# Kernel tuning notes

Hardware: AMD Instinct MI355X
Metric: run time of the kernel (lower is better)

## Reference

```python
import jax, jax.numpy as jnp
import numpy as np

HIDDEN = 768
NUM_BLOCKS = 8
BLOCK = HIDDEN // NUM_BLOCKS  # 96
HSF = 1                       # hidden_size_factor
LAMBDA = 0.01                 # softshrink threshold
SCALE = 0.02


def setup_inputs() -> dict:
    key = jax.random.key(0)
    ks = jax.random.split(key, 9)
    B, C, N = 16, HIDDEN, 4096
    x = jax.random.normal(ks[0], (B, C, N), dtype=jnp.float32)
    u = lambda k, shp: SCALE * jax.random.uniform(k, shp, dtype=jnp.float32)
    OB = BLOCK * HSF
    return {
        'x': x,
        'w1_re': u(ks[1], (NUM_BLOCKS, BLOCK, OB)),
        'w1_im': u(ks[2], (NUM_BLOCKS, BLOCK, OB)),
        'w2_re': u(ks[3], (NUM_BLOCKS, OB, BLOCK)),
        'w2_im': u(ks[4], (NUM_BLOCKS, OB, BLOCK)),
        'b1_re': u(ks[5], (NUM_BLOCKS, OB)),
        'b1_im': u(ks[6], (NUM_BLOCKS, OB)),
        'b2_re': u(ks[7], (NUM_BLOCKS, BLOCK)),
        'b2_im': u(ks[8], (NUM_BLOCKS, BLOCK)),
    }


def _softshrink(v, lam):
    return jnp.sign(v) * jnp.maximum(jnp.abs(v) - lam, 0.0)


def _crelu(z):
    # activation applied to view_as_real, i.e. independently on re/im
    return jax.lax.complex(jnp.maximum(z.real, 0.0), jnp.maximum(z.imag, 0.0))


def reference(x, w1_re, w1_im, w2_re, w2_im, b1_re, b1_im, b2_re, b2_im):
    B, C, N = x.shape
    bias = x
    w1 = jax.lax.complex(w1_re, w1_im)
    w2 = jax.lax.complex(w2_re, w2_im)
    b1 = jax.lax.complex(b1_re, b1_im)
    b2 = jax.lax.complex(b2_re, b2_im)

    xf = jnp.fft.rfft(x.astype(jnp.float32), norm='ortho')   # [B, C, M], M = N//2+1
    M = xf.shape[-1]
    xf = xf.reshape(B, NUM_BLOCKS, BLOCK, M)                  # [B, nb, bs, M]

    # kept_modes == M since hard_thresholding_fraction == 1
    h = jnp.einsum('bnim,nio->bnom', xf, w1) + b1[None, :, :, None]
    h = _crelu(h)
    o = jnp.einsum('bnim,nio->bnom', h, w2) + b2[None, :, :, None]
    o = jax.lax.complex(_softshrink(o.real, LAMBDA), _softshrink(o.imag, LAMBDA))

    o = o.reshape(B, C, M)
    y = jnp.fft.irfft(o, n=N, norm='ortho').astype(x.dtype)
    return y + bias
```

## Files before the change

kernel.cpp:

```cpp
#include <hip/hip_runtime.h>
#include <math.h>

#define NTH 256
#define LAM 0.01f
#define WS_WT_BYTES 589824

typedef __attribute__((ext_vector_type(8))) short short8;
typedef __attribute__((ext_vector_type(8))) unsigned short ushort8;
typedef __attribute__((ext_vector_type(4))) float f32x4;
typedef __attribute__((ext_vector_type(4))) unsigned int uint4v;

__device__ __forceinline__ ushort f2bf(float f) {
    union { float f; unsigned u; } c; c.f = f;
    unsigned u = c.u;
    u += 0x7fffu + ((u >> 16) & 1u);
    return (ushort)(u >> 16);
}
__device__ __forceinline__ float bf2f(ushort h) {
    union { unsigned u; float f; } c; c.u = ((unsigned)h) << 16; return c.f;
}


__device__ __forceinline__ int pad(int i) { return i + (i >> 3); }
#define FFT_LDS_SZ 2304

__device__ __forceinline__ float2 cadd(float2 a, float2 b) { return make_float2(a.x + b.x, a.y + b.y); }
__device__ __forceinline__ float2 csub(float2 a, float2 b) { return make_float2(a.x - b.x, a.y - b.y); }
__device__ __forceinline__ float2 cmul(float2 a, float2 b) { return make_float2(a.x * b.x - a.y * b.y, a.x * b.y + a.y * b.x); }
__device__ __forceinline__ float2 cjrot(float2 a, float sign) { return make_float2(-sign * a.y, sign * a.x); }

__device__ __forceinline__ void radix8_bfly(const float2 t[8], float2 o[8], float sign) {
    float2 apc = cadd(t[0], t[4]), amc = csub(t[0], t[4]);
    float2 bpd = cadd(t[2], t[6]), bmd = csub(t[2], t[6]);
    float2 e0 = cadd(apc, bpd), e2 = csub(apc, bpd);
    float2 jb = cjrot(bmd, sign);
    float2 e1 = cadd(amc, jb), e3 = csub(amc, jb);
    float2 apc2 = cadd(t[1], t[5]), amc2 = csub(t[1], t[5]);
    float2 bpd2 = cadd(t[3], t[7]), bmd2 = csub(t[3], t[7]);
    float2 q0 = cadd(apc2, bpd2), q2 = csub(apc2, bpd2);
    float2 jb2 = cjrot(bmd2, sign);
    float2 q1 = cadd(amc2, jb2), q3 = csub(amc2, jb2);
    const float H = 0.70710678118654752f;
    q1 = cmul(q1, make_float2(H, sign * H));
    q2 = cjrot(q2, sign);
    q3 = cmul(q3, make_float2(-H, sign * H));
    o[0] = cadd(e0, q0); o[1] = cadd(e1, q1); o[2] = cadd(e2, q2); o[3] = cadd(e3, q3);
    o[4] = csub(e0, q0); o[5] = csub(e1, q1); o[6] = csub(e2, q2); o[7] = csub(e3, q3);
}

__device__ __forceinline__ void radix8_stage(const float2* __restrict__ src,
                                             float2* __restrict__ dst,
                                             int tid, int Ns, float sign) {
    const int u = tid;
    const int r = u & (Ns - 1);
    float2 t[8];
    t[0] = src[pad(u)];
    t[1] = src[pad(u + 256)];
    t[2] = src[pad(u + 512)];
    t[3] = src[pad(u + 768)];
    t[4] = src[pad(u + 1024)];
    t[5] = src[pad(u + 1280)];
    t[6] = src[pad(u + 1536)];
    t[7] = src[pad(u + 1792)];
    {
        float ang = sign * ((float)M_PI / (4.0f * (float)Ns)) * (float)r;
        float s1, c1;
        __sincosf(ang, &s1, &c1);
        float2 w1 = make_float2(c1, s1);
        float2 w2 = cmul(w1, w1);
        float2 w3 = cmul(w2, w1);
        float2 w4 = cmul(w2, w2);
        float2 w5 = cmul(w4, w1);
        float2 w6 = cmul(w4, w2);
        float2 w7 = cmul(w4, w3);
        t[1] = cmul(t[1], w1); t[2] = cmul(t[2], w2); t[3] = cmul(t[3], w3);
        t[4] = cmul(t[4], w4); t[5] = cmul(t[5], w5); t[6] = cmul(t[6], w6);
        t[7] = cmul(t[7], w7);
    }
    float2 o[8];
    radix8_bfly(t, o, sign);
    const int d = ((u - r) << 3) + r;
    dst[pad(d)]          = o[0];
    dst[pad(d + Ns)]     = o[1];
    dst[pad(d + 2 * Ns)] = o[2];
    dst[pad(d + 3 * Ns)] = o[3];
    dst[pad(d + 4 * Ns)] = o[4];
    dst[pad(d + 5 * Ns)] = o[5];
    dst[pad(d + 6 * Ns)] = o[6];
    dst[pad(d + 7 * Ns)] = o[7];
}

__device__ __forceinline__ void radix4_final(const float2* __restrict__ src,
                                             float2* __restrict__ dst,
                                             int tid, float sign) {
    for (int u = tid; u < 512; u += NTH) {
        float2 x0 = src[pad(u)];
        float2 x1 = src[pad(u + 512)];
        float2 x2 = src[pad(u + 1024)];
        float2 x3 = src[pad(u + 1536)];
        float ang = sign * ((float)M_PI / 1024.0f) * (float)u;
        float s1, c1;
        __sincosf(ang, &s1, &c1);
        float2 w1 = make_float2(c1, s1);
        float2 w2 = cmul(w1, w1);
        float2 w3 = cmul(w2, w1);
        x1 = cmul(x1, w1); x2 = cmul(x2, w2); x3 = cmul(x3, w3);
        float2 apc = cadd(x0, x2), amc = csub(x0, x2);
        float2 bpd = cadd(x1, x3), bmd = csub(x1, x3);
        float2 e = cjrot(bmd, sign);
        dst[pad(u)]        = cadd(apc, bpd);
        dst[pad(u + 512)]  = cadd(amc, e);
        dst[pad(u + 1024)] = csub(apc, bpd);
        dst[pad(u + 1536)] = csub(amc, e);
    }
}

__global__ __launch_bounds__(NTH, 4) void k_rfft_fwd(const float* __restrict__ x,
                                                     float* __restrict__ out) {
    __shared__ float2 bufA[FFT_LDS_SZ];
    __shared__ float2 bufB[FFT_LDS_SZ];
    const int row = blockIdx.x;
    const float* xr = x + (size_t)row * 4096;
    unsigned* srow = (unsigned*)(out + (size_t)row * 4096);
    const int tid = threadIdx.x;

    {
        float2 t[8], o[8];
#pragma unroll
        for (int j = 0; j < 8; ++j)
            t[j] = *(const float2*)(xr + 2 * (tid + 256 * j));
        radix8_bfly(t, o, -1.0f);
#pragma unroll
        for (int j = 0; j < 8; ++j)
            bufB[pad(8 * tid + j)] = o[j];
    }
    __syncthreads();
    radix8_stage(bufB, bufA, tid, 8, -1.0f);
    __syncthreads();
    radix8_stage(bufA, bufB, tid, 64, -1.0f);
    __syncthreads();
    radix4_final(bufB, bufA, tid, -1.0f);
    __syncthreads();
    float2* Z = bufA;

    const float scale = 1.0f / 64.0f;
    float s0, c0;
    __sincosf(-(float)M_PI * (float)tid / 2048.0f, &s0, &c0);
    float2 w = make_float2(c0, s0);
    const float2 stepw = make_float2(0.92387953251128674f, -0.38268343236508978f);
    for (int k = tid; k <= 2048; k += NTH) {
        float2 zk = Z[pad(k & 2047)];
        float2 zn = Z[pad((2048 - k) & 2047)];
        float Ar = 0.5f * (zk.x + zn.x), Ai = 0.5f * (zk.y - zn.y);
        float Br = 0.5f * (zk.x - zn.x), Bi = 0.5f * (zk.y + zn.y);
        float wBr = w.x * Br - w.y * Bi;
        float wBi = w.x * Bi + w.y * Br;
        float Xr = (Ar + wBi) * scale;
        float Xi = (Ai - wBr) * scale;
        if (k == 0)          ((ushort*)srow)[0] = f2bf(Xr);
        else if (k == 2048)  ((ushort*)srow)[1] = f2bf(Xr);
        else                 srow[k] = (unsigned)f2bf(Xr) | ((unsigned)f2bf(Xi) << 16);
        w = cmul(w, stepw);
    }
}

__global__ __launch_bounds__(NTH) void k_prep(
    const float* __restrict__ w1_re, const float* __restrict__ w1_im,
    const float* __restrict__ w2_re, const float* __restrict__ w2_im,
    ushort* __restrict__ wt) {
    int gid = blockIdx.x * NTH + threadIdx.x;
    if (gid >= 294912) return;
    int a   = gid / 73728;
    int rem = gid - a * 73728;
    int n   = rem / 9216;
    int r2  = rem - n * 9216;
    int o   = r2 / 96;
    int i   = r2 - o * 96;
    const float* src = (a == 0) ? w1_re : (a == 1) ? w1_im : (a == 2) ? w2_re : w2_im;
    wt[gid] = f2bf(src[(n * 96 + i) * 96 + o]);
}

__global__ __launch_bounds__(NTH, 3) void k_mix6(
    float* __restrict__ io, const ushort* __restrict__ wt,
    const float* __restrict__ b1_re, const float* __restrict__ b1_im,
    const float* __restrict__ b2_re, const float* __restrict__ b2_im) {
    __shared__ __align__(16) ushort xb[2][64][104];

    const int mt = blockIdx.x;
    const int n  = blockIdx.y;
    const int b  = blockIdx.z;
    const int tid  = threadIdx.x;
    const int lane = tid & 63;
    const int wv   = tid >> 6;
    const int m0 = mt * 64;
    const int mw = wv * 16;
    unsigned* sb = (unsigned*)(io + ((size_t)b * 768 + (size_t)n * 96) * 4096);

    const int lc = lane & 15;
    const int hi = lane >> 4;

    {
        const int m = m0 + mw + lc;
        if (m >= 1 && m < 2048) {
            const unsigned* src0 = sb + m;
#pragma unroll
            for (int half = 0; half < 2; ++half) {
                unsigned v[12];
#pragma unroll
                for (int t = 0; t < 12; ++t) {
                    const int i = hi + 4 * (12 * half + t);
                    v[t] = src0[(size_t)i * 4096];
                }
#pragma unroll
                for (int t = 0; t < 12; ++t) {
                    const int i = hi + 4 * (12 * half + t);
                    xb[0][mw + lc][i] = (ushort)v[t];
                    xb[1][mw + lc][i] = (ushort)(v[t] >> 16);
                }
            }
        } else {
            for (int i = hi; i < 96; i += 4) {
                const ushort* rw = (const ushort*)(sb + (size_t)i * 4096);
                ushort re16 = 0;
                if (m == 0)          re16 = rw[0];
                else if (m == 2048)  re16 = rw[1];
                xb[0][mw + lc][i] = re16;
                xb[1][mw + lc][i] = 0;
            }
        }
    }

    const int kl = 8 * hi;
    const int mrow = mw + lc;
    const ushort* wn  = wt + (size_t)n * 9216;
    const ushort* wn2 = wn + 2 * 73728;

    float b1r[6], b1i[6];
#pragma unroll
    for (int nt = 0; nt < 6; ++nt) {
        b1r[nt] = b1_re[n * 96 + nt * 16 + lc];
        b1i[nt] = b1_im[n * 96 + nt * 16 + lc];
    }

    f32x4 accR[6], accI[6];
    const f32x4 zero = {0.f, 0.f, 0.f, 0.f};
#pragma unroll
    for (int nt = 0; nt < 6; ++nt) { accR[nt] = zero; accI[nt] = zero; }

#pragma unroll
    for (int kk = 0; kk < 3; ++kk) {
        const int k0 = kk * 32 + kl;
        short8 wr[6], wi[6];
#pragma unroll
        for (int nt = 0; nt < 6; ++nt) {
            const ushort* wp = wn + (nt * 16 + lc) * 96 + k0;
            wr[nt] = *(const short8*)(wp);
            wi[nt] = *(const short8*)(wp + 73728);
        }
        short8 ar = *(const short8*)&xb[0][mrow][k0];
        short8 ai = *(const short8*)&xb[1][mrow][k0];
        short8 nai;
#pragma unroll
        for (int j = 0; j < 8; ++j) nai[j] = ai[j] ^ (short)0x8000;
#pragma unroll
        for (int nt = 0; nt < 6; ++nt) {
            accR[nt] = __builtin_amdgcn_mfma_f32_16x16x32_bf16(ar,  wr[nt], accR[nt], 0, 0, 0);
            accR[nt] = __builtin_amdgcn_mfma_f32_16x16x32_bf16(nai, wi[nt], accR[nt], 0, 0, 0);
            accI[nt] = __builtin_amdgcn_mfma_f32_16x16x32_bf16(ar,  wi[nt], accI[nt], 0, 0, 0);
            accI[nt] = __builtin_amdgcn_mfma_f32_16x16x32_bf16(ai,  wr[nt], accI[nt], 0, 0, 0);
        }
    }
#pragma unroll
    for (int nt = 0; nt < 6; ++nt) {
#pragma unroll
        for (int q = 0; q < 4; ++q) {
            int m = mw + 4 * hi + q;
            xb[0][m][nt * 16 + lc] = f2bf(fmaxf(accR[nt][q] + b1r[nt], 0.f));
            xb[1][m][nt * 16 + lc] = f2bf(fmaxf(accI[nt][q] + b1i[nt], 0.f));
        }
    }

#pragma unroll
    for (int nt = 0; nt < 6; ++nt) { accR[nt] = zero; accI[nt] = zero; }
#pragma unroll
    for (int kk = 0; kk < 3; ++kk) {
        const int k0 = kk * 32 + kl;
        short8 wr[6], wi[6];
#pragma unroll
        for (int nt = 0; nt < 6; ++nt) {
            const ushort* wp = wn2 + (nt * 16 + lc) * 96 + k0;
            wr[nt] = *(const short8*)(wp);
            wi[nt] = *(const short8*)(wp + 73728);
        }
        short8 ar = *(const short8*)&xb[0][mrow][k0];
        short8 ai = *(const short8*)&xb[1][mrow][k0];
        short8 nai;
#pragma unroll
        for (int j = 0; j < 8; ++j) nai[j] = ai[j] ^ (short)0x8000;
#pragma unroll
        for (int nt = 0; nt < 6; ++nt) {
            accR[nt] = __builtin_amdgcn_mfma_f32_16x16x32_bf16(ar,  wr[nt], accR[nt], 0, 0, 0);
            accR[nt] = __builtin_amdgcn_mfma_f32_16x16x32_bf16(nai, wi[nt], accR[nt], 0, 0, 0);
            accI[nt] = __builtin_amdgcn_mfma_f32_16x16x32_bf16(ar,  wi[nt], accI[nt], 0, 0, 0);
            accI[nt] = __builtin_amdgcn_mfma_f32_16x16x32_bf16(ai,  wr[nt], accI[nt], 0, 0, 0);
        }
    }

    float b2r[6], b2i[6];
#pragma unroll
    for (int nt = 0; nt < 6; ++nt) {
        b2r[nt] = b2_re[n * 96 + nt * 16 + lc];
        b2i[nt] = b2_im[n * 96 + nt * 16 + lc];
    }
    const int mq = m0 + mw + 4 * hi;
#pragma unroll
    for (int nt = 0; nt < 6; ++nt) {
        float sr[4], si[4];
#pragma unroll
        for (int q = 0; q < 4; ++q) {
            float vr = accR[nt][q] + b2r[nt];
            float vi = accI[nt][q] + b2i[nt];
            sr[q] = copysignf(fmaxf(fabsf(vr) - LAM, 0.f), vr);
            si[q] = copysignf(fmaxf(fabsf(vi) - LAM, 0.f), vi);
        }
        unsigned* row = sb + (size_t)(nt * 16 + lc) * 4096;
        if (mq >= 1 && mq + 3 < 2048) {
            uint4v pk;
#pragma unroll
            for (int q = 0; q < 4; ++q)
                pk[q] = (unsigned)f2bf(sr[q]) | ((unsigned)f2bf(si[q]) << 16);
            *(uint4v*)(row + mq) = pk;
        } else {
#pragma unroll
            for (int q = 0; q < 4; ++q) {
                int m = mq + q;
                if (m == 0)          ((ushort*)row)[0] = f2bf(sr[q]);
                else if (m == 2048)  ((ushort*)row)[1] = f2bf(sr[q]);
                else if (m < 2048)   row[m] = (unsigned)f2bf(sr[q]) | ((unsigned)f2bf(si[q]) << 16);
            }
        }
    }
}

__global__ __launch_bounds__(NTH) void k_mix_fallback(
    float* __restrict__ io,
    const float* __restrict__ w1_re, const float* __restrict__ w1_im,
    const float* __restrict__ w2_re, const float* __restrict__ w2_im,
    const float* __restrict__ b1_re, const float* __restrict__ b1_im,
    const float* __restrict__ b2_re, const float* __restrict__ b2_im) {
    __shared__ __align__(16) ushort xb[2][64][96];
    __shared__ __align__(16) ushort wb[2][96][104];

    const int mt = blockIdx.x;
    const int n  = blockIdx.y;
    const int b  = blockIdx.z;
    const int tid = threadIdx.x;
    const int lane = tid & 63;
    const int wv   = tid >> 6;
    const int m0 = mt * 64;
    unsigned* sb = (unsigned*)(io + ((size_t)b * 768 + (size_t)n * 96) * 4096);

    for (int idx = tid; idx < 96 * 64; idx += NTH) {
        int i = idx >> 6, mm = idx & 63;
        int m = m0 + mm;
        const unsigned* row = sb + (size_t)i * 4096;
        ushort re = 0, im = 0;
        if (m == 0) { re = ((const ushort*)row)[0]; }
        else if (m == 2048) { re = ((const ushort*)row)[1]; }
        else if (m < 2048) { unsigned v = row[m]; re = (ushort)v; im = (ushort)(v >> 16); }
        xb[0][mm][i] = re;
        xb[1][mm][i] = im;
    }
    const float* W1r = w1_re + (size_t)n * 9216;
    const float* W1i = w1_im + (size_t)n * 9216;
    for (int idx = tid; idx < 9216; idx += NTH) {
        int i = idx / 96, o = idx - i * 96;
        wb[0][o][i] = f2bf(W1r[idx]);
        wb[1][o][i] = f2bf(W1i[idx]);
    }
    const int lc = lane & 15;
    float b1r[6], b1i[6], b2r[6], b2i[6];
#pragma unroll
    for (int nt = 0; nt < 6; ++nt) {
        b1r[nt] = b1_re[n * 96 + nt * 16 + lc];
        b1i[nt] = b1_im[n * 96 + nt * 16 + lc];
        b2r[nt] = b2_re[n * 96 + nt * 16 + lc];
        b2i[nt] = b2_im[n * 96 + nt * 16 + lc];
    }
    __syncthreads();

    const int mw = wv * 16;
    const int klr = 8 * (lane >> 4);
    const int mrow = mw + lc;

    f32x4 accR[6], accI[6];
    const f32x4 zero = {0.f, 0.f, 0.f, 0.f};
#pragma unroll
    for (int nt = 0; nt < 6; ++nt) { accR[nt] = zero; accI[nt] = zero; }

#pragma unroll
    for (int kk = 0; kk < 3; ++kk) {
        int k0 = kk * 32 + klr;
        short8 ar = *(const short8*)&xb[0][mrow][k0];
        short8 ai = *(const short8*)&xb[1][mrow][k0];
        short8 nai;
#pragma unroll
        for (int j = 0; j < 8; ++j) nai[j] = ai[j] ^ (short)0x8000;
#pragma unroll
        for (int nt = 0; nt < 6; ++nt) {
            short8 br = *(const short8*)&wb[0][nt * 16 + lc][k0];
            short8 bi = *(const short8*)&wb[1][nt * 16 + lc][k0];
            accR[nt] = __builtin_amdgcn_mfma_f32_16x16x32_bf16(ar,  br, accR[nt], 0, 0, 0);
            accR[nt] = __builtin_amdgcn_mfma_f32_16x16x32_bf16(nai, bi, accR[nt], 0, 0, 0);
            accI[nt] = __builtin_amdgcn_mfma_f32_16x16x32_bf16(ar,  bi, accI[nt], 0, 0, 0);
            accI[nt] = __builtin_amdgcn_mfma_f32_16x16x32_bf16(ai,  br, accI[nt], 0, 0, 0);
        }
    }
#pragma unroll
    for (int nt = 0; nt < 6; ++nt) {
#pragma unroll
        for (int q = 0; q < 4; ++q) {
            int m = mw + 4 * (lane >> 4) + q;
            float hr = fmaxf(accR[nt][q] + b1r[nt], 0.f);
            float hi2 = fmaxf(accI[nt][q] + b1i[nt], 0.f);
            xb[0][m][nt * 16 + lc] = f2bf(hr);
            xb[1][m][nt * 16 + lc] = f2bf(hi2);
        }
    }
    __syncthreads();

    const float* W2r = w2_re + (size_t)n * 9216;
    const float* W2i = w2_im + (size_t)n * 9216;
    for (int idx = tid; idx < 9216; idx += NTH) {
        int i = idx / 96, o = idx - i * 96;
        wb[0][o][i] = f2bf(W2r[idx]);
        wb[1][o][i] = f2bf(W2i[idx]);
    }
    __syncthreads();

#pragma unroll
    for (int nt = 0; nt < 6; ++nt) { accR[nt] = zero; accI[nt] = zero; }
#pragma unroll
    for (int kk = 0; kk < 3; ++kk) {
        int k0 = kk * 32 + klr;
        short8 ar = *(const short8*)&xb[0][mrow][k0];
        short8 ai = *(const short8*)&xb[1][mrow][k0];
        short8 nai;
#pragma unroll
        for (int j = 0; j < 8; ++j) nai[j] = ai[j] ^ (short)0x8000;
#pragma unroll
        for (int nt = 0; nt < 6; ++nt) {
            short8 br = *(const short8*)&wb[0][nt * 16 + lc][k0];
            short8 bi = *(const short8*)&wb[1][nt * 16 + lc][k0];
            accR[nt] = __builtin_amdgcn_mfma_f32_16x16x32_bf16(ar,  br, accR[nt], 0, 0, 0);
            accR[nt] = __builtin_amdgcn_mfma_f32_16x16x32_bf16(nai, bi, accR[nt], 0, 0, 0);
            accI[nt] = __builtin_amdgcn_mfma_f32_16x16x32_bf16(ar,  bi, accI[nt], 0, 0, 0);
            accI[nt] = __builtin_amdgcn_mfma_f32_16x16x32_bf16(ai,  br, accI[nt], 0, 0, 0);
        }
    }
#pragma unroll
    for (int nt = 0; nt < 6; ++nt) {
#pragma unroll
        for (int q = 0; q < 4; ++q) {
            int m = m0 + mw + 4 * (lane >> 4) + q;
            float vr = accR[nt][q] + b2r[nt];
            float vi = accI[nt][q] + b2i[nt];
            float sr = copysignf(fmaxf(fabsf(vr) - LAM, 0.f), vr);
            float si = copysignf(fmaxf(fabsf(vi) - LAM, 0.f), vi);
            unsigned* row = sb + (size_t)(nt * 16 + lc) * 4096;
            if (m == 0)          ((ushort*)row)[0] = f2bf(sr);
            else if (m == 2048)  ((ushort*)row)[1] = f2bf(sr);
            else if (m < 2048)   row[m] = (unsigned)f2bf(sr) | ((unsigned)f2bf(si) << 16);
        }
    }
}

__global__ __launch_bounds__(NTH, 4) void k_irfft_add(const float* __restrict__ x,
                                                      float* __restrict__ io) {
    __shared__ float2 bufA[FFT_LDS_SZ];
    __shared__ float2 bufB[FFT_LDS_SZ];
    const int row = blockIdx.x;
    const float* xr = x + (size_t)row * 4096;
    float* orow = io + (size_t)row * 4096;
    const unsigned* srow = (const unsigned*)orow;
    const int tid = threadIdx.x;
    const float scale = 1.0f / 32.0f;

    {
        float2 t[8], o[8];
        float s0, c0;
        __sincosf((float)M_PI * (float)tid / 2048.0f, &s0, &c0);
        float2 w = make_float2(c0, s0);
        const float2 stepw = make_float2(0.92387953251128674f, 0.38268343236508978f);
#pragma unroll
        for (int j = 0; j < 8; ++j) {
            const int k = tid + 256 * j;
            float Xr, Xi, Yr, Yi;
            if (k == 0) {
                unsigned v0 = srow[0];
                Xr = bf2f((ushort)v0); Xi = 0.f;
                Yr = bf2f((ushort)(v0 >> 16)); Yi = 0.f;
            } else {
                unsigned a  = srow[k];
                unsigned bq = srow[2048 - k];
                Xr = bf2f((ushort)a);  Xi = bf2f((ushort)(a >> 16));
                Yr = bf2f((ushort)bq); Yi = bf2f((ushort)(bq >> 16));
            }
            float Fer = 0.5f * (Xr + Yr), Fei = 0.5f * (Xi - Yi);
            float Dr  = 0.5f * (Xr - Yr), Di  = 0.5f * (Xi + Yi);
            float For = w.x * Dr - w.y * Di;
            float Foi = w.x * Di + w.y * Dr;
            t[j] = make_float2((Fer - Foi) * scale, (Fei + For) * scale);
            w = cmul(w, stepw);
        }
        radix8_bfly(t, o, 1.0f);
#pragma unroll
        for (int j = 0; j < 8; ++j)
            bufB[pad(8 * tid + j)] = o[j];
    }
    __syncthreads();
    radix8_stage(bufB, bufA, tid, 8, 1.0f);
    __syncthreads();
    radix8_stage(bufA, bufB, tid, 64, 1.0f);
    __syncthreads();

#pragma unroll
    for (int it = 0; it < 2; ++it) {
        const int u = tid + 256 * it;
        float2 x0 = bufB[pad(u)];
        float2 x1 = bufB[pad(u + 512)];
        float2 x2 = bufB[pad(u + 1024)];
        float2 x3 = bufB[pad(u + 1536)];
        float ang = ((float)M_PI / 1024.0f) * (float)u;
        float s1, c1;
        __sincosf(ang, &s1, &c1);
        float2 w1 = make_float2(c1, s1);
        float2 w2 = cmul(w1, w1);
        float2 w3 = cmul(w2, w1);
        x1 = cmul(x1, w1); x2 = cmul(x2, w2); x3 = cmul(x3, w3);
        float2 apc = cadd(x0, x2), amc = csub(x0, x2);
        float2 bpd = cadd(x1, x3), bmd = csub(x1, x3);
        float2 e = cjrot(bmd, 1.0f);
        float2 y0 = cadd(apc, bpd);
        float2 y1 = cadd(amc, e);
        float2 y2 = csub(apc, bpd);
        float2 y3 = csub(amc, e);
        float2 xv0 = *(const float2*)(xr + 2 * u);
        float2 xv1 = *(const float2*)(xr + 2 * (u + 512));
        float2 xv2 = *(const float2*)(xr + 2 * (u + 1024));
        float2 xv3 = *(const float2*)(xr + 2 * (u + 1536));
        *(float2*)(orow + 2 * u)          = cadd(y0, xv0);
        *(float2*)(orow + 2 * (u + 512))  = cadd(y1, xv1);
        *(float2*)(orow + 2 * (u + 1024)) = cadd(y2, xv2);
        *(float2*)(orow + 2 * (u + 1536)) = cadd(y3, xv3);
    }
}

extern "C" void kernel_launch(void* const* d_in, const int* in_sizes, int n_in,
                              void* d_out, int out_size, void* d_ws, size_t ws_size,
                              hipStream_t stream) {
    const float* x     = (const float*)d_in[0];
    const float* w1_re = (const float*)d_in[1];
    const float* w1_im = (const float*)d_in[2];
    const float* w2_re = (const float*)d_in[3];
    const float* w2_im = (const float*)d_in[4];
    const float* b1_re = (const float*)d_in[5];
    const float* b1_im = (const float*)d_in[6];
    const float* b2_re = (const float*)d_in[7];
    const float* b2_im = (const float*)d_in[8];
    float* out = (float*)d_out;

    k_rfft_fwd<<<12288, NTH, 0, stream>>>(x, out);
    if (ws_size >= (size_t)WS_WT_BYTES) {
        ushort* wt = (ushort*)d_ws;
        k_prep<<<(294912 + NTH - 1) / NTH, NTH, 0, stream>>>(w1_re, w1_im, w2_re, w2_im, wt);
        k_mix6<<<dim3(33, 8, 16), NTH, 0, stream>>>(out, wt, b1_re, b1_im, b2_re, b2_im);
    } else {
        k_mix_fallback<<<dim3(33, 8, 16), NTH, 0, stream>>>(out, w1_re, w1_im, w2_re, w2_im,
                                                            b1_re, b1_im, b2_re, b2_im);
    }
    k_irfft_add<<<12288, NTH, 0, stream>>>(x, out);
}
```

Before: 263.6 us.

## Process three m-tiles per block with register prefetch of the next tile

```diff
diff --git a/kernel.cpp b/kernel.cpp
--- a/kernel.cpp
+++ b/kernel.cpp
@@ -180,56 +180,23 @@
     wt[gid] = f2bf(src[(n * 96 + i) * 96 + o]);
 }
 
-__global__ __launch_bounds__(NTH, 3) void k_mix6(
+__global__ __launch_bounds__(NTH, 3) void k_mix7(
     float* __restrict__ io, const ushort* __restrict__ wt,
     const float* __restrict__ b1_re, const float* __restrict__ b1_im,
     const float* __restrict__ b2_re, const float* __restrict__ b2_im) {
     __shared__ __align__(16) ushort xb[2][64][104];
 
-    const int mt = blockIdx.x;
+    const int gx = blockIdx.x;
     const int n  = blockIdx.y;
     const int b  = blockIdx.z;
     const int tid  = threadIdx.x;
     const int lane = tid & 63;
     const int wv   = tid >> 6;
-    const int m0 = mt * 64;
     const int mw = wv * 16;
     unsigned* sb = (unsigned*)(io + ((size_t)b * 768 + (size_t)n * 96) * 4096);
 
     const int lc = lane & 15;
     const int hi = lane >> 4;
-
-    {
-        const int m = m0 + mw + lc;
-        if (m >= 1 && m < 2048) {
-            const unsigned* src0 = sb + m;
-#pragma unroll
-            for (int half = 0; half < 2; ++half) {
-                unsigned v[12];
-#pragma unroll
-                for (int t = 0; t < 12; ++t) {
-                    const int i = hi + 4 * (12 * half + t);
-                    v[t] = src0[(size_t)i * 4096];
-                }
-#pragma unroll
-                for (int t = 0; t < 12; ++t) {
-                    const int i = hi + 4 * (12 * half + t);
-                    xb[0][mw + lc][i] = (ushort)v[t];
-                    xb[1][mw + lc][i] = (ushort)(v[t] >> 16);
-                }
-            }
-        } else {
-            for (int i = hi; i < 96; i += 4) {
-                const ushort* rw = (const ushort*)(sb + (size_t)i * 4096);
-                ushort re16 = 0;
-                if (m == 0)          re16 = rw[0];
-                else if (m == 2048)  re16 = rw[1];
-                xb[0][mw + lc][i] = re16;
-                xb[1][mw + lc][i] = 0;
-            }
-        }
-    }
-
     const int kl = 8 * hi;
     const int mrow = mw + lc;
     const ushort* wn  = wt + (size_t)n * 9216;
@@ -242,101 +209,137 @@
         b1i[nt] = b1_im[n * 96 + nt * 16 + lc];
     }
 
-    f32x4 accR[6], accI[6];
+    unsigned vA[24];
+    {
+        const int m = gx * 192 + mw + lc;
+        const unsigned* src0 = sb + ((m >= 1 && m < 2048) ? m : 0);
+#pragma unroll
+        for (int t = 0; t < 24; ++t)
+            vA[t] = src0[(size_t)(hi + 4 * t) * 4096];
+    }
+
     const f32x4 zero = {0.f, 0.f, 0.f, 0.f};
-#pragma unroll
-    for (int nt = 0; nt < 6; ++nt) { accR[nt] = zero; accI[nt] = zero; }
-
-#pragma unroll
-    for (int kk = 0; kk < 3; ++kk) {
-        const int k0 = kk * 32 + kl;
-        short8 wr[6], wi[6];
+
+#pragma unroll
+    for (int j = 0; j < 3; ++j) {
+        const int m0 = (gx * 3 + j) * 64;
+        const int m  = m0 + mw + lc;
+        {
+            const bool interior = (m >= 1 && m < 2048);
+#pragma unroll
+            for (int t = 0; t < 24; ++t) {
+                const int i = hi + 4 * t;
+                unsigned v = vA[t];
+                ushort lo = (ushort)v, h16 = (ushort)(v >> 16);
+                ushort re = (m == 2048) ? h16 : (m < 2048 ? lo : (ushort)0);
+                ushort im = interior ? h16 : (ushort)0;
+                xb[0][mw + lc][i] = re;
+                xb[1][mw + lc][i] = im;
+            }
+        }
+        if (j < 2) {
+            const int mn = m0 + 64 + mw + lc;
+            const unsigned* src0 = sb + ((mn >= 1 && mn < 2048) ? mn : 0);
+#pragma unroll
+            for (int t = 0; t < 24; ++t)
+                vA[t] = src0[(size_t)(hi + 4 * t) * 4096];
+        }
+
+        f32x4 accR[6], accI[6];
+#pragma unroll
+        for (int nt = 0; nt < 6; ++nt) { accR[nt] = zero; accI[nt] = zero; }
+
+#pragma unroll
+        for (int kk = 0; kk < 3; ++kk) {
+            const int k0 = kk * 32 + kl;
+            short8 wr[6], wi[6];
+#pragma unroll
+            for (int nt = 0; nt < 6; ++nt) {
+                const ushort* wp = wn + (nt * 16 + lc) * 96 + k0;
+                wr[nt] = *(const short8*)(wp);
+                wi[nt] = *(const short8*)(wp + 73728);
+            }
+            short8 ar = *(const short8*)&xb[0][mrow][k0];
+            short8 ai = *(const short8*)&xb[1][mrow][k0];
+            short8 nai;
+#pragma unroll
+            for (int jj = 0; jj < 8; ++jj) nai[jj] = ai[jj] ^ (short)0x8000;
+#pragma unroll
+            for (int nt = 0; nt < 6; ++nt) {
+                accR[nt] = __builtin_amdgcn_mfma_f32_16x16x32_bf16(ar,  wr[nt], accR[nt], 0, 0, 0);
+                accR[nt] = __builtin_amdgcn_mfma_f32_16x16x32_bf16(nai, wi[nt], accR[nt], 0, 0, 0);
+                accI[nt] = __builtin_amdgcn_mfma_f32_16x16x32_bf16(ar,  wi[nt], accI[nt], 0, 0, 0);
+                accI[nt] = __builtin_amdgcn_mfma_f32_16x16x32_bf16(ai,  wr[nt], accI[nt], 0, 0, 0);
+            }
+        }
 #pragma unroll
         for (int nt = 0; nt < 6; ++nt) {
-            const ushort* wp = wn + (nt * 16 + lc) * 96 + k0;
-            wr[nt] = *(const short8*)(wp);
-            wi[nt] = *(const short8*)(wp + 73728);
-        }
-        short8 ar = *(const short8*)&xb[0][mrow][k0];
-        short8 ai = *(const short8*)&xb[1][mrow][k0];
-        short8 nai;
-#pragma unroll
-        for (int j = 0; j < 8; ++j) nai[j] = ai[j] ^ (short)0x8000;
+#pragma unroll
+            for (int q = 0; q < 4; ++q) {
+                int mm = mw + 4 * hi + q;
+                xb[0][mm][nt * 16 + lc] = f2bf(fmaxf(accR[nt][q] + b1r[nt], 0.f));
+                xb[1][mm][nt * 16 + lc] = f2bf(fmaxf(accI[nt][q] + b1i[nt], 0.f));
+            }
+        }
+
+#pragma unroll
+        for (int nt = 0; nt < 6; ++nt) { accR[nt] = zero; accI[nt] = zero; }
+#pragma unroll
+        for (int kk = 0; kk < 3; ++kk) {
+            const int k0 = kk * 32 + kl;
+            short8 wr[6], wi[6];
+#pragma unroll
+            for (int nt = 0; nt < 6; ++nt) {
+                const ushort* wp = wn2 + (nt * 16 + lc) * 96 + k0;
+                wr[nt] = *(const short8*)(wp);
+                wi[nt] = *(const short8*)(wp + 73728);
+            }
+            short8 ar = *(const short8*)&xb[0][mrow][k0];
+            short8 ai = *(const short8*)&xb[1][mrow][k0];
+            short8 nai;
+#pragma unroll
+            for (int jj = 0; jj < 8; ++jj) nai[jj] = ai[jj] ^ (short)0x8000;
+#pragma unroll
+            for (int nt = 0; nt < 6; ++nt) {
+                accR[nt] = __builtin_amdgcn_mfma_f32_16x16x32_bf16(ar,  wr[nt], accR[nt], 0, 0, 0);
+                accR[nt] = __builtin_amdgcn_mfma_f32_16x16x32_bf16(nai, wi[nt], accR[nt], 0, 0, 0);
+                accI[nt] = __builtin_amdgcn_mfma_f32_16x16x32_bf16(ar,  wi[nt], accI[nt], 0, 0, 0);
+                accI[nt] = __builtin_amdgcn_mfma_f32_16x16x32_bf16(ai,  wr[nt], accI[nt], 0, 0, 0);
+            }
+        }
+
+        float b2r[6], b2i[6];
 #pragma unroll
         for (int nt = 0; nt < 6; ++nt) {
-            accR[nt] = __builtin_amdgcn_mfma_f32_16x16x32_bf16(ar,  wr[nt], accR[nt], 0, 0, 0);
-            accR[nt] = __builtin_amdgcn_mfma_f32_16x16x32_bf16(nai, wi[nt], accR[nt], 0, 0, 0);
-            accI[nt] = __builtin_amdgcn_mfma_f32_16x16x32_bf16(ar,  wi[nt], accI[nt], 0, 0, 0);
-            accI[nt] = __builtin_amdgcn_mfma_f32_16x16x32_bf16(ai,  wr[nt], accI[nt], 0, 0, 0);
-        }
-    }
-#pragma unroll
-    for (int nt = 0; nt < 6; ++nt) {
-#pragma unroll
-        for (int q = 0; q < 4; ++q) {
-            int m = mw + 4 * hi + q;
-            xb[0][m][nt * 16 + lc] = f2bf(fmaxf(accR[nt][q] + b1r[nt], 0.f));
-            xb[1][m][nt * 16 + lc] = f2bf(fmaxf(accI[nt][q] + b1i[nt], 0.f));
-        }
-    }
-
-#pragma unroll
-    for (int nt = 0; nt < 6; ++nt) { accR[nt] = zero; accI[nt] = zero; }
-#pragma unroll
-    for (int kk = 0; kk < 3; ++kk) {
-        const int k0 = kk * 32 + kl;
-        short8 wr[6], wi[6];
+            b2r[nt] = b2_re[n * 96 + nt * 16 + lc];
+            b2i[nt] = b2_im[n * 96 + nt * 16 + lc];
+        }
+        const int mq = m0 + mw + 4 * hi;
 #pragma unroll
         for (int nt = 0; nt < 6; ++nt) {
-            const ushort* wp = wn2 + (nt * 16 + lc) * 96 + k0;
-            wr[nt] = *(const short8*)(wp);
-            wi[nt] = *(const short8*)(wp + 73728);
-        }
-        short8 ar = *(const short8*)&xb[0][mrow][k0];
-        short8 ai = *(const short8*)&xb[1][mrow][k0];
-        short8 nai;
-#pragma unroll
-        for (int j = 0; j < 8; ++j) nai[j] = ai[j] ^ (short)0x8000;
-#pragma unroll
-        for (int nt = 0; nt < 6; ++nt) {
-            accR[nt] = __builtin_amdgcn_mfma_f32_16x16x32_bf16(ar,  wr[nt], accR[nt], 0, 0, 0);
-            accR[nt] = __builtin_amdgcn_mfma_f32_16x16x32_bf16(nai, wi[nt], accR[nt], 0, 0, 0);
-            accI[nt] = __builtin_amdgcn_mfma_f32_16x16x32_bf16(ar,  wi[nt], accI[nt], 0, 0, 0);
-            accI[nt] = __builtin_amdgcn_mfma_f32_16x16x32_bf16(ai,  wr[nt], accI[nt], 0, 0, 0);
-        }
-    }
-
-    float b2r[6], b2i[6];
-#pragma unroll
-    for (int nt = 0; nt < 6; ++nt) {
-        b2r[nt] = b2_re[n * 96 + nt * 16 + lc];
-        b2i[nt] = b2_im[n * 96 + nt * 16 + lc];
-    }
-    const int mq = m0 + mw + 4 * hi;
-#pragma unroll
-    for (int nt = 0; nt < 6; ++nt) {
-        float sr[4], si[4];
-#pragma unroll
-        for (int q = 0; q < 4; ++q) {
-            float vr = accR[nt][q] + b2r[nt];
-            float vi = accI[nt][q] + b2i[nt];
-            sr[q] = copysignf(fmaxf(fabsf(vr) - LAM, 0.f), vr);
-            si[q] = copysignf(fmaxf(fabsf(vi) - LAM, 0.f), vi);
-        }
-        unsigned* row = sb + (size_t)(nt * 16 + lc) * 4096;
-        if (mq >= 1 && mq + 3 < 2048) {
-            uint4v pk;
-#pragma unroll
-            for (int q = 0; q < 4; ++q)
-                pk[q] = (unsigned)f2bf(sr[q]) | ((unsigned)f2bf(si[q]) << 16);
-            *(uint4v*)(row + mq) = pk;
-        } else {
+            float sr[4], si[4];
 #pragma unroll
             for (int q = 0; q < 4; ++q) {
-                int m = mq + q;
-                if (m == 0)          ((ushort*)row)[0] = f2bf(sr[q]);
-                else if (m == 2048)  ((ushort*)row)[1] = f2bf(sr[q]);
-                else if (m < 2048)   row[m] = (unsigned)f2bf(sr[q]) | ((unsigned)f2bf(si[q]) << 16);
+                float vr = accR[nt][q] + b2r[nt];
+                float vi = accI[nt][q] + b2i[nt];
+                sr[q] = copysignf(fmaxf(fabsf(vr) - LAM, 0.f), vr);
+                si[q] = copysignf(fmaxf(fabsf(vi) - LAM, 0.f), vi);
+            }
+            unsigned* row = sb + (size_t)(nt * 16 + lc) * 4096;
+            if (mq >= 1 && mq + 3 < 2048) {
+                uint4v pk;
+#pragma unroll
+                for (int q = 0; q < 4; ++q)
+                    pk[q] = (unsigned)f2bf(sr[q]) | ((unsigned)f2bf(si[q]) << 16);
+                *(uint4v*)(row + mq) = pk;
+            } else {
+#pragma unroll
+                for (int q = 0; q < 4; ++q) {
+                    int mm = mq + q;
+                    if (mm == 0)          ((ushort*)row)[0] = f2bf(sr[q]);
+                    else if (mm == 2048)  ((ushort*)row)[1] = f2bf(sr[q]);
+                    else if (mm < 2048)   row[mm] = (unsigned)f2bf(sr[q]) | ((unsigned)f2bf(si[q]) << 16);
+                }
             }
         }
     }
@@ -574,7 +577,7 @@
     if (ws_size >= (size_t)WS_WT_BYTES) {
         ushort* wt = (ushort*)d_ws;
         k_prep<<<(294912 + NTH - 1) / NTH, NTH, 0, stream>>>(w1_re, w1_im, w2_re, w2_im, wt);
-        k_mix6<<<dim3(33, 8, 16), NTH, 0, stream>>>(out, wt, b1_re, b1_im, b2_re, b2_im);
+        k_mix7<<<dim3(11, 8, 16), NTH, 0, stream>>>(out, wt, b1_re, b1_im, b2_re, b2_im);
     } else {
         k_mix_fallback<<<dim3(33, 8, 16), NTH, 0, stream>>>(out, w1_re, w1_im, w2_re, w2_im,
                                                             b1_re, b1_im, b2_re, b2_im);
```

Result: slower. 380.2 us (+44.2%).

## Give each mix wavefront two 16-row tiles to reuse weight fragments

Applied to the files above, without the earlier changes.

```diff
diff --git a/kernel.cpp b/kernel.cpp
--- a/kernel.cpp
+++ b/kernel.cpp
@@ -2,6 +2,7 @@
 #include <math.h>
 
 #define NTH 256
+#define NTHM 128
 #define LAM 0.01f
 #define WS_WT_BYTES 589824
 
@@ -180,7 +181,7 @@
     wt[gid] = f2bf(src[(n * 96 + i) * 96 + o]);
 }
 
-__global__ __launch_bounds__(NTH, 3) void k_mix6(
+__global__ __launch_bounds__(NTHM, 2) void k_mix9(
     float* __restrict__ io, const ushort* __restrict__ wt,
     const float* __restrict__ b1_re, const float* __restrict__ b1_im,
     const float* __restrict__ b2_re, const float* __restrict__ b2_im) {
@@ -193,14 +194,16 @@
     const int lane = tid & 63;
     const int wv   = tid >> 6;
     const int m0 = mt * 64;
-    const int mw = wv * 16;
+    const int ws0 = wv * 32;
     unsigned* sb = (unsigned*)(io + ((size_t)b * 768 + (size_t)n * 96) * 4096);
 
     const int lc = lane & 15;
     const int hi = lane >> 4;
 
-    {
-        const int m = m0 + mw + lc;
+#pragma unroll
+    for (int t2 = 0; t2 < 2; ++t2) {
+        const int mrow = ws0 + t2 * 16 + lc;
+        const int m = m0 + mrow;
         if (m >= 1 && m < 2048) {
             const unsigned* src0 = sb + m;
 #pragma unroll
@@ -214,8 +217,8 @@
 #pragma unroll
                 for (int t = 0; t < 12; ++t) {
                     const int i = hi + 4 * (12 * half + t);
-                    xb[0][mw + lc][i] = (ushort)v[t];
-                    xb[1][mw + lc][i] = (ushort)(v[t] >> 16);
+                    xb[0][mrow][i] = (ushort)v[t];
+                    xb[1][mrow][i] = (ushort)(v[t] >> 16);
                 }
             }
         } else {
@@ -224,14 +227,15 @@
                 ushort re16 = 0;
                 if (m == 0)          re16 = rw[0];
                 else if (m == 2048)  re16 = rw[1];
-                xb[0][mw + lc][i] = re16;
-                xb[1][mw + lc][i] = 0;
+                xb[0][mrow][i] = re16;
+                xb[1][mrow][i] = 0;
             }
         }
     }
 
     const int kl = 8 * hi;
-    const int mrow = mw + lc;
+    const int mr0 = ws0 + lc;
+    const int mr1 = ws0 + 16 + lc;
     const ushort* wn  = wt + (size_t)n * 9216;
     const ushort* wn2 = wn + 2 * 73728;
 
@@ -242,10 +246,12 @@
         b1i[nt] = b1_im[n * 96 + nt * 16 + lc];
     }
 
-    f32x4 accR[6], accI[6];
+    f32x4 accR[2][6], accI[2][6];
     const f32x4 zero = {0.f, 0.f, 0.f, 0.f};
 #pragma unroll
-    for (int nt = 0; nt < 6; ++nt) { accR[nt] = zero; accI[nt] = zero; }
+    for (int t2 = 0; t2 < 2; ++t2)
+#pragma unroll
+        for (int nt = 0; nt < 6; ++nt) { accR[t2][nt] = zero; accI[t2][nt] = zero; }
 
 #pragma unroll
     for (int kk = 0; kk < 3; ++kk) {
@@ -257,31 +263,41 @@
             wr[nt] = *(const short8*)(wp);
             wi[nt] = *(const short8*)(wp + 73728);
         }
-        short8 ar = *(const short8*)&xb[0][mrow][k0];
-        short8 ai = *(const short8*)&xb[1][mrow][k0];
-        short8 nai;
-#pragma unroll
-        for (int j = 0; j < 8; ++j) nai[j] = ai[j] ^ (short)0x8000;
-#pragma unroll
-        for (int nt = 0; nt < 6; ++nt) {
-            accR[nt] = __builtin_amdgcn_mfma_f32_16x16x32_bf16(ar,  wr[nt], accR[nt], 0, 0, 0);
-            accR[nt] = __builtin_amdgcn_mfma_f32_16x16x32_bf16(nai, wi[nt], accR[nt], 0, 0, 0);
-            accI[nt] = __builtin_amdgcn_mfma_f32_16x16x32_bf16(ar,  wi[nt], accI[nt], 0, 0, 0);
-            accI[nt] = __builtin_amdgcn_mfma_f32_16x16x32_bf16(ai,  wr[nt], accI[nt], 0, 0, 0);
-        }
-    }
-#pragma unroll
-    for (int nt = 0; nt < 6; ++nt) {
-#pragma unroll
-        for (int q = 0; q < 4; ++q) {
-            int m = mw + 4 * hi + q;
-            xb[0][m][nt * 16 + lc] = f2bf(fmaxf(accR[nt][q] + b1r[nt], 0.f));
-            xb[1][m][nt * 16 + lc] = f2bf(fmaxf(accI[nt][q] + b1i[nt], 0.f));
-        }
-    }
-
-#pragma unroll
-    for (int nt = 0; nt < 6; ++nt) { accR[nt] = zero; accI[nt] = zero; }
+        short8 arA = *(const short8*)&xb[0][mr0][k0];
+        short8 aiA = *(const short8*)&xb[1][mr0][k0];
+        short8 arB = *(const short8*)&xb[0][mr1][k0];
+        short8 aiB = *(const short8*)&xb[1][mr1][k0];
+        short8 naiA, naiB;
+#pragma unroll
+        for (int j = 0; j < 8; ++j) { naiA[j] = aiA[j] ^ (short)0x8000; naiB[j] = aiB[j] ^ (short)0x8000; }
+#pragma unroll
+        for (int nt = 0; nt < 6; ++nt) {
+            accR[0][nt] = __builtin_amdgcn_mfma_f32_16x16x32_bf16(arA,  wr[nt], accR[0][nt], 0, 0, 0);
+            accR[0][nt] = __builtin_amdgcn_mfma_f32_16x16x32_bf16(naiA, wi[nt], accR[0][nt], 0, 0, 0);
+            accI[0][nt] = __builtin_amdgcn_mfma_f32_16x16x32_bf16(arA,  wi[nt], accI[0][nt], 0, 0, 0);
+            accI[0][nt] = __builtin_amdgcn_mfma_f32_16x16x32_bf16(aiA,  wr[nt], accI[0][nt], 0, 0, 0);
+            accR[1][nt] = __builtin_amdgcn_mfma_f32_16x16x32_bf16(arB,  wr[nt], accR[1][nt], 0, 0, 0);
+            accR[1][nt] = __builtin_amdgcn_mfma_f32_16x16x32_bf16(naiB, wi[nt], accR[1][nt], 0, 0, 0);
+            accI[1][nt] = __builtin_amdgcn_mfma_f32_16x16x32_bf16(arB,  wi[nt], accI[1][nt], 0, 0, 0);
+            accI[1][nt] = __builtin_amdgcn_mfma_f32_16x16x32_bf16(aiB,  wr[nt], accI[1][nt], 0, 0, 0);
+        }
+    }
+#pragma unroll
+    for (int t2 = 0; t2 < 2; ++t2)
+#pragma unroll
+        for (int nt = 0; nt < 6; ++nt) {
+#pragma unroll
+            for (int q = 0; q < 4; ++q) {
+                int mm = ws0 + t2 * 16 + 4 * hi + q;
+                xb[0][mm][nt * 16 + lc] = f2bf(fmaxf(accR[t2][nt][q] + b1r[nt], 0.f));
+                xb[1][mm][nt * 16 + lc] = f2bf(fmaxf(accI[t2][nt][q] + b1i[nt], 0.f));
+            }
+        }
+
+#pragma unroll
+    for (int t2 = 0; t2 < 2; ++t2)
+#pragma unroll
+        for (int nt = 0; nt < 6; ++nt) { accR[t2][nt] = zero; accI[t2][nt] = zero; }
 #pragma unroll
     for (int kk = 0; kk < 3; ++kk) {
         const int k0 = kk * 32 + kl;
@@ -292,17 +308,23 @@
             wr[nt] = *(const short8*)(wp);
             wi[nt] = *(const short8*)(wp + 73728);
         }
-        short8 ar = *(const short8*)&xb[0][mrow][k0];
-        short8 ai = *(const short8*)&xb[1][mrow][k0];
-        short8 nai;
-#pragma unroll
-        for (int j = 0; j < 8; ++j) nai[j] = ai[j] ^ (short)0x8000;
-#pragma unroll
-        for (int nt = 0; nt < 6; ++nt) {
-            accR[nt] = __builtin_amdgcn_mfma_f32_16x16x32_bf16(ar,  wr[nt], accR[nt], 0, 0, 0);
-            accR[nt] = __builtin_amdgcn_mfma_f32_16x16x32_bf16(nai, wi[nt], accR[nt], 0, 0, 0);
-            accI[nt] = __builtin_amdgcn_mfma_f32_16x16x32_bf16(ar,  wi[nt], accI[nt], 0, 0, 0);
-            accI[nt] = __builtin_amdgcn_mfma_f32_16x16x32_bf16(ai,  wr[nt], accI[nt], 0, 0, 0);
+        short8 arA = *(const short8*)&xb[0][mr0][k0];
+        short8 aiA = *(const short8*)&xb[1][mr0][k0];
+        short8 arB = *(const short8*)&xb[0][mr1][k0];
+        short8 aiB = *(const short8*)&xb[1][mr1][k0];
+        short8 naiA, naiB;
+#pragma unroll
+        for (int j = 0; j < 8; ++j) { naiA[j] = aiA[j] ^ (short)0x8000; naiB[j] = aiB[j] ^ (short)0x8000; }
+#pragma unroll
+        for (int nt = 0; nt < 6; ++nt) {
+            accR[0][nt] = __builtin_amdgcn_mfma_f32_16x16x32_bf16(arA,  wr[nt], accR[0][nt], 0, 0, 0);
+            accR[0][nt] = __builtin_amdgcn_mfma_f32_16x16x32_bf16(naiA, wi[nt], accR[0][nt], 0, 0, 0);
+            accI[0][nt] = __builtin_amdgcn_mfma_f32_16x16x32_bf16(arA,  wi[nt], accI[0][nt], 0, 0, 0);
+            accI[0][nt] = __builtin_amdgcn_mfma_f32_16x16x32_bf16(aiA,  wr[nt], accI[0][nt], 0, 0, 0);
+            accR[1][nt] = __builtin_amdgcn_mfma_f32_16x16x32_bf16(arB,  wr[nt], accR[1][nt], 0, 0, 0);
+            accR[1][nt] = __builtin_amdgcn_mfma_f32_16x16x32_bf16(naiB, wi[nt], accR[1][nt], 0, 0, 0);
+            accI[1][nt] = __builtin_amdgcn_mfma_f32_16x16x32_bf16(arB,  wi[nt], accI[1][nt], 0, 0, 0);
+            accI[1][nt] = __builtin_amdgcn_mfma_f32_16x16x32_bf16(aiB,  wr[nt], accI[1][nt], 0, 0, 0);
         }
     }
 
@@ -312,31 +334,34 @@
         b2r[nt] = b2_re[n * 96 + nt * 16 + lc];
         b2i[nt] = b2_im[n * 96 + nt * 16 + lc];
     }
-    const int mq = m0 + mw + 4 * hi;
-#pragma unroll
-    for (int nt = 0; nt < 6; ++nt) {
-        float sr[4], si[4];
-#pragma unroll
-        for (int q = 0; q < 4; ++q) {
-            float vr = accR[nt][q] + b2r[nt];
-            float vi = accI[nt][q] + b2i[nt];
-            sr[q] = copysignf(fmaxf(fabsf(vr) - LAM, 0.f), vr);
-            si[q] = copysignf(fmaxf(fabsf(vi) - LAM, 0.f), vi);
-        }
-        unsigned* row = sb + (size_t)(nt * 16 + lc) * 4096;
-        if (mq >= 1 && mq + 3 < 2048) {
-            uint4v pk;
-#pragma unroll
-            for (int q = 0; q < 4; ++q)
-                pk[q] = (unsigned)f2bf(sr[q]) | ((unsigned)f2bf(si[q]) << 16);
-            *(uint4v*)(row + mq) = pk;
-        } else {
+#pragma unroll
+    for (int t2 = 0; t2 < 2; ++t2) {
+        const int mq = m0 + ws0 + t2 * 16 + 4 * hi;
+#pragma unroll
+        for (int nt = 0; nt < 6; ++nt) {
+            float sr[4], si[4];
 #pragma unroll
             for (int q = 0; q < 4; ++q) {
-                int m = mq + q;
-                if (m == 0)          ((ushort*)row)[0] = f2bf(sr[q]);
-                else if (m == 2048)  ((ushort*)row)[1] = f2bf(sr[q]);
-                else if (m < 2048)   row[m] = (unsigned)f2bf(sr[q]) | ((unsigned)f2bf(si[q]) << 16);
+                float vr = accR[t2][nt][q] + b2r[nt];
+                float vi = accI[t2][nt][q] + b2i[nt];
+                sr[q] = copysignf(fmaxf(fabsf(vr) - LAM, 0.f), vr);
+                si[q] = copysignf(fmaxf(fabsf(vi) - LAM, 0.f), vi);
+            }
+            unsigned* row = sb + (size_t)(nt * 16 + lc) * 4096;
+            if (mq >= 1 && mq + 3 < 2048) {
+                uint4v pk;
+#pragma unroll
+                for (int q = 0; q < 4; ++q)
+                    pk[q] = (unsigned)f2bf(sr[q]) | ((unsigned)f2bf(si[q]) << 16);
+                *(uint4v*)(row + mq) = pk;
+            } else {
+#pragma unroll
+                for (int q = 0; q < 4; ++q) {
+                    int m = mq + q;
+                    if (m == 0)          ((ushort*)row)[0] = f2bf(sr[q]);
+                    else if (m == 2048)  ((ushort*)row)[1] = f2bf(sr[q]);
+                    else if (m < 2048)   row[m] = (unsigned)f2bf(sr[q]) | ((unsigned)f2bf(si[q]) << 16);
+                }
             }
         }
     }
@@ -574,7 +599,7 @@
     if (ws_size >= (size_t)WS_WT_BYTES) {
         ushort* wt = (ushort*)d_ws;
         k_prep<<<(294912 + NTH - 1) / NTH, NTH, 0, stream>>>(w1_re, w1_im, w2_re, w2_im, wt);
-        k_mix6<<<dim3(33, 8, 16), NTH, 0, stream>>>(out, wt, b1_re, b1_im, b2_re, b2_im);
+        k_mix9<<<dim3(33, 8, 16), NTHM, 0, stream>>>(out, wt, b1_re, b1_im, b2_re, b2_im);
     } else {
         k_mix_fallback<<<dim3(33, 8, 16), NTH, 0, stream>>>(out, w1_re, w1_im, w2_re, w2_im,
                                                             b1_re, b1_im, b2_re, b2_im);
```

Result: faster. 256.9 us (-2.5%).
